# Kernel optimization log

Measured on AMD Instinct MI355X. Metric: run time of the kernel, lower is better.

## Reference

```python
import jax, jax.numpy as jnp
import numpy as np

_OFF = 8
_M = 512  # coordinate hash base (> max coord + 2*_OFF)

def _enc(c):
    c64 = c.astype(np.int64) + _OFF
    return (c64[:, 0] * _M + c64[:, 1]) * _M + c64[:, 2]

def _kmap(out_c, in_c, scale):
    """Per-offset neighbor map: maps[k, j] = index into in_c of voxel out_c[j] + scale*offset_k, or -1."""
    ik = _enc(in_c)
    order = np.argsort(ik)
    sk = ik[order]
    maps = np.full((27, len(out_c)), -1, np.int32)
    k = 0
    for dx in (-1, 0, 1):
        for dy in (-1, 0, 1):
            for dz in (-1, 0, 1):
                ck = _enc(out_c + np.array([dx, dy, dz]) * scale)
                pos = np.clip(np.searchsorted(sk, ck), 0, len(sk) - 1)
                hit = sk[pos] == ck
                maps[k] = np.where(hit, order[pos].astype(np.int32), -1)
                k += 1
    return maps


def setup_inputs() -> dict:
    rng = np.random.default_rng(0)
    c = rng.integers(0, 160, size=(300000, 3))
    c0 = np.unique(c, axis=0)[:200000]          # stride-1 voxels
    c2 = np.unique((c0 // 2) * 2, axis=0)       # stride-2 voxels
    c4 = np.unique((c2 // 4) * 4, axis=0)       # stride-4 voxels

    maps = {
        'map0':  jnp.asarray(_kmap(c0, c0, 1)),   # block0  (s=1)
        'map1':  jnp.asarray(_kmap(c2, c0, 1)),   # block1  (s=2 down)
        'map2':  jnp.asarray(_kmap(c4, c2, 2)),   # block2  (s=2 down)
        'map2t': jnp.asarray(_kmap(c2, c4, 2)),   # block2_tr (transposed)
        'map1t': jnp.asarray(_kmap(c0, c2, 1)),   # block1_tr (transposed)
        'map0t': jnp.asarray(_kmap(c0, c0, 1)),   # block0_tr (s=1)
    }

    key = jax.random.key(0)
    ks = jax.random.split(key, 8)

    def w(k, cin, cout):
        return jax.random.normal(k, (27, cin, cout), jnp.float32) / np.sqrt(27.0 * cin)

    nf, e = 16, 32
    inp = {'feats': jax.random.normal(ks[0], (c0.shape[0], nf), jnp.float32)}
    inp['W0'] = w(ks[1], nf, e);          inp['g0'] = jnp.ones((e,));        inp['b0'] = jnp.zeros((e,))
    inp['W1'] = w(ks[2], e, 2 * e);       inp['g1'] = jnp.ones((2 * e,));    inp['b1'] = jnp.zeros((2 * e,))
    inp['W2'] = w(ks[3], 2 * e, 4 * e);   inp['g2'] = jnp.ones((4 * e,));    inp['b2'] = jnp.zeros((4 * e,))
    inp['W2t'] = w(ks[4], 4 * e, 2 * e);  inp['g2t'] = jnp.ones((2 * e,));   inp['b2t'] = jnp.zeros((2 * e,))
    inp['W1t'] = w(ks[5], 4 * e, 2 * e);  inp['g1t'] = jnp.ones((2 * e,));   inp['b1t'] = jnp.zeros((2 * e,))
    inp['W0t'] = w(ks[6], 3 * e, 2)
    inp.update(maps)
    return inp


def _sconv(x, W, m):
    """Sparse 3D conv as gather-GEMM-scatter. x:[Nin,Cin], W:[27,Cin,Cout], m:[27,Nout]."""
    valid = m >= 0
    idx = jnp.maximum(m, 0)
    acc0 = jnp.zeros((m.shape[1], W.shape[2]), x.dtype)

    def body(acc, kw):
        mk, vk, Wk = kw
        g = jnp.where(vk[:, None], x[mk], 0.0)
        return acc + g @ Wk, None

    out, _ = jax.lax.scan(body, acc0, (idx, valid, W))
    return out


def _bn_relu(x, g, b, eps=1e-5):
    mu = x.mean(0)
    var = x.var(0)
    return jax.nn.relu((x - mu) * jax.lax.rsqrt(var + eps) * g + b)


def reference(feats, W0, g0, b0, W1, g1, b1, W2, g2, b2,
              W2t, g2t, b2t, W1t, g1t, b1t, W0t,
              map0, map1, map2, map2t, map1t, map0t):
    s1 = _bn_relu(_sconv(feats, W0, map0), g0, b0)   # [N0, 32]
    s2 = _bn_relu(_sconv(s1, W1, map1), g1, b1)      # [N1, 64]
    s4 = _bn_relu(_sconv(s2, W2, map2), g2, b2)      # [N2, 128]
    d2 = _bn_relu(_sconv(s4, W2t, map2t), g2t, b2t)  # [N1, 64]
    d2 = jnp.concatenate([d2, s2], axis=1)           # [N1, 128] skip cat
    d1 = _bn_relu(_sconv(d2, W1t, map1t), g1t, b1t)  # [N0, 64]
    d1 = jnp.concatenate([d1, s1], axis=1)           # [N0, 96] skip cat
    return _sconv(d1, W0t, map0t)                    # [N0, 2]
```

## Files before the change

kernel.cpp:

```cpp
#include <hip/hip_runtime.h>
#include <cstddef>
#include <cstdint>

#define BN_EPS 1e-5f

typedef float f2 __attribute__((ext_vector_type(2)));
typedef float f4 __attribute__((ext_vector_type(4)));
typedef float f32x4 __attribute__((ext_vector_type(4)));
typedef _Float16 h2 __attribute__((ext_vector_type(2)));
typedef _Float16 h8 __attribute__((ext_vector_type(8)));

__device__ __forceinline__ int xcd_swz(int bid, int nwg)
{
    const int q = nwg >> 3, r = nwg & 7;
    const int xcd = bid & 7, idx = bid >> 3;
    const int base = (xcd < r) ? xcd * (q + 1) : r * (q + 1) + (xcd - r) * q;
    return base + idx;
}

template<int CIN, int COUT>
__global__ __launch_bounds__(256)
void wtrans_mf(const float* __restrict__ W, _Float16* __restrict__ Wm)
{
    constexpr int NT = CIN / 32;
    constexpr int NC = COUT / 16;
    const int t = blockIdx.x * 256 + threadIdx.x;
    constexpr int TOTAL = 27 * NT * NC * 64;
    if (t >= TOTAL) return;
    const int lane = t & 63;
    int rest = t >> 6;
    const int ct = rest % NC; rest /= NC;
    const int tt = rest % NT;
    const int k  = rest / NT;
    const int cin0 = tt * 32 + (lane >> 4) * 8;
    const int co   = ct * 16 + (lane & 15);
    h8 v;
    #pragma unroll
    for (int u = 0; u < 8; ++u)
        v[u] = (_Float16)W[((size_t)k * CIN + cin0 + u) * COUT + co];
    *(h8*)(Wm + (size_t)t * 8) = v;
}

__global__ __launch_bounds__(256)
void wtrans_mf0(const float* __restrict__ W, _Float16* __restrict__ Wm0)
{
    const int t = blockIdx.x * 256 + threadIdx.x;
    constexpr int TOTAL = 27 * 2 * 32;
    if (t >= TOTAL) return;
    const int co = t % 32;
    const int s  = (t / 32) % 2;
    const int k  = t / 64;
    h8 v;
    #pragma unroll
    for (int u = 0; u < 8; ++u)
        v[u] = (_Float16)W[((size_t)k * 16 + s * 8 + u) * 32 + co];
    *(h8*)(Wm0 + (size_t)t * 8) = v;
}

__global__ __launch_bounds__(256)
void map_transpose_cls(const int* __restrict__ map, int Nout,
                       int* __restrict__ mapT, unsigned char* __restrict__ cls,
                       int* __restrict__ counts)
{
    __shared__ int s[256][28];
    __shared__ int hist[9];
    const int tid  = threadIdx.x;
    const int base = blockIdx.x * 256;
    const int j    = base + tid;
    if (tid < 9) hist[tid] = 0;
    for (int k = 0; k < 27; ++k)
        s[tid][k] = (j < Nout) ? map[(size_t)k * Nout + j] : -1;
    __syncthreads();
    for (int i = tid; i < 256 * 32; i += 256) {
        const int r = i >> 5, c = i & 31;
        if (base + r < Nout)
            mapT[(size_t)(base + r) * 32 + c] = (c < 27) ? s[r][c] : -1;
    }
    if (j < Nout) {
        int c9 = 8;
        #pragma unroll 1
        for (int k = 0; k < 27; ++k) {
            if (s[tid][k] >= 0) {
                const int dz = k % 3, dy = (k / 3) % 3, dx = k / 9;
                c9 = ((dx != 1) << 2) | ((dy != 1) << 1) | (int)(dz != 1);
                break;
            }
        }
        cls[j] = (unsigned char)c9;
        atomicAdd(&hist[c9], 1);
    }
    __syncthreads();
    if (tid < 9 && hist[tid] > 0)
        atomicAdd(&counts[tid], hist[tid]);
}

__global__ __launch_bounds__(256)
void scatter_compact(const unsigned char* __restrict__ cls, int Nout,
                     const int* __restrict__ counts, int* __restrict__ cursors,
                     int* __restrict__ order)
{
    __shared__ int hist[9], basec[9];
    const int tid = threadIdx.x;
    const int j   = blockIdx.x * 256 + tid;
    if (tid < 9) hist[tid] = 0;
    const int c9 = (j < Nout) ? (int)cls[j] : -1;
    __syncthreads();
    int lpos = 0;
    if (c9 >= 0) lpos = atomicAdd(&hist[c9], 1);
    __syncthreads();
    if (tid < 9 && hist[tid] > 0)
        basec[tid] = atomicAdd(&cursors[tid], hist[tid]);
    __syncthreads();
    if (c9 >= 0) {
        int offs = 0;
        #pragma unroll
        for (int c = 0; c < 9; ++c)
            if (c < c9) offs += counts[c];
        order[offs + basec[c9] + lpos] = j;
    }
}

__global__ __launch_bounds__(256)
void sconv_mf0(const float* __restrict__ x, const _Float16* __restrict__ Wm0,
               const int* __restrict__ map, int Nout,
               _Float16* __restrict__ out, const float* __restrict__ zrow)
{
    const int lane = threadIdx.x & 63;
    const int wave = threadIdx.x >> 6;
    const int row0 = (blockIdx.x * 4 + wave) * 16;

    __shared__ int smap[4][16][28];

    int mk[16];
    bool anyv = false;
    #pragma unroll
    for (int r = 0; r < 16; ++r) {
        const int j = row0 + r;
        mk[r] = (lane < 27 && j < Nout) ? map[(size_t)lane * Nout + j] : -1;
        anyv |= (mk[r] >= 0);
    }
    unsigned long long act = __ballot(anyv);

    if (lane < 27) {
        #pragma unroll
        for (int r = 0; r < 16; ++r)
            smap[wave][r][lane] = mk[r];
    }

    f32x4 accH[2], accL[2];
    #pragma unroll
    for (int c = 0; c < 2; ++c) {
        accH[c] = (f32x4){0.f, 0.f, 0.f, 0.f};
        accL[c] = (f32x4){0.f, 0.f, 0.f, 0.f};
    }

    const int rrow = lane & 15;
    const int kseg = lane >> 4;
    const int half = kseg & 1;
    const bool useK1 = (kseg < 2);

    while (act) {
        const int k1 = (int)__builtin_ctzll(act);
        act &= act - 1;
        int k2 = -1;
        if (act) {
            k2 = (int)__builtin_ctzll(act);
            act &= act - 1;
        }
        const int ks = useK1 ? k1 : k2;
        int m = -1;
        if (ks >= 0) m = smap[wave][rrow][ks];

        const float* px = (m >= 0) ? (x + (size_t)m * 16 + half * 8)
                                   : (zrow + half * 8);
        const f4 x0 = *(const f4*)px;
        const f4 x1 = *(const f4*)(px + 4);
        h8 aH, aL;
        #pragma unroll
        for (int u = 0; u < 4; ++u) {
            const float v0 = x0[u], v1 = x1[u];
            const _Float16 h0 = (_Float16)v0;
            const _Float16 h1 = (_Float16)v1;
            aH[u]     = h0;
            aH[u + 4] = h1;
            aL[u]     = (_Float16)((v0 - (float)h0) * 2048.f);
            aL[u + 4] = (_Float16)((v1 - (float)h1) * 2048.f);
        }

        const int ksafe = (ks >= 0) ? ks : 0;
        const _Float16* wb = Wm0 + ((size_t)(ksafe * 2 + half) * 32) * 8;
        #pragma unroll
        for (int c = 0; c < 2; ++c) {
            const h8 b = *(const h8*)(wb + (size_t)(c * 16 + rrow) * 8);
            accH[c] = __builtin_amdgcn_mfma_f32_16x16x32_f16(aH, b, accH[c], 0, 0, 0);
            accL[c] = __builtin_amdgcn_mfma_f32_16x16x32_f16(aL, b, accL[c], 0, 0, 0);
        }
    }

    #pragma unroll
    for (int c = 0; c < 2; ++c) {
        #pragma unroll
        for (int r = 0; r < 4; ++r) {
            const int j = row0 + kseg * 4 + r;
            if (j < Nout)
                out[(size_t)j * 32 + c * 16 + rrow] =
                    (_Float16)(accH[c][r] + accL[c][r] * (1.f / 2048.f));
        }
    }
}

template<int CIN, int CINA, int COUT>
__global__ __launch_bounds__(256)
void sconv_mf(const _Float16* __restrict__ xA, const _Float16* __restrict__ xB,
              const _Float16* __restrict__ Wm, const int* __restrict__ map,
              int Nout, _Float16* __restrict__ out,
              const _Float16* __restrict__ zrh)
{
    constexpr int CINB = CIN - CINA;
    constexpr int NT = CIN / 32;
    constexpr int NC = COUT / 16;
    static_assert(CINA % 32 == 0, "CINA must be a multiple of 32");
    const int lane = threadIdx.x & 63;
    const int wave = threadIdx.x >> 6;
    const int row0 = (blockIdx.x * 4 + wave) * 32;

    __shared__ int smap[4][32][28];

    int mv[32];
    #pragma unroll
    for (int r = 0; r < 32; ++r) {
        const int j = row0 + r;
        mv[r] = (lane < 27 && j < Nout) ? map[(size_t)lane * Nout + j] : -1;
    }
    bool anyv = false;
    #pragma unroll
    for (int r = 0; r < 32; ++r) {
        if (lane < 27) smap[wave][r][lane] = mv[r];
        anyv |= (mv[r] >= 0);
    }
    unsigned long long act = __ballot(anyv) & 0x7FFFFFFull;

    f32x4 acc[2][NC];
    #pragma unroll
    for (int tt = 0; tt < 2; ++tt)
        #pragma unroll
        for (int c = 0; c < NC; ++c) acc[tt][c] = (f32x4){0.f, 0.f, 0.f, 0.f};

    const int rrow = lane & 15;
    const int kseg = lane >> 4;

    auto loada = [&](int k, h8 a[2][NT]) {
        #pragma unroll
        for (int tt = 0; tt < 2; ++tt) {
            const int m = smap[wave][tt * 16 + rrow][k];
            #pragma unroll
            for (int t = 0; t < NT; ++t) {
                const int cin0 = t * 32 + kseg * 8;
                const _Float16* pa;
                if (m >= 0) {
                    if (CINB > 0 && t * 32 >= CINA)
                        pa = xB + (size_t)m * CINB + (cin0 - CINA);
                    else
                        pa = xA + (size_t)m * CINA + cin0;
                } else {
                    pa = zrh;
                }
                a[tt][t] = *(const h8*)pa;
            }
        }
    };
    auto compute = [&](int k, h8 a[2][NT]) {
        const _Float16* Wk = Wm + ((size_t)k * NT * NC * 64 + lane) * 8;
        #pragma unroll
        for (int t = 0; t < NT; ++t) {
            #pragma unroll
            for (int c = 0; c < NC; ++c) {
                const h8 b = *(const h8*)(Wk + (size_t)(t * NC + c) * 64 * 8);
                acc[0][c] = __builtin_amdgcn_mfma_f32_16x16x32_f16(a[0][t], b, acc[0][c], 0, 0, 0);
                acc[1][c] = __builtin_amdgcn_mfma_f32_16x16x32_f16(a[1][t], b, acc[1][c], 0, 0, 0);
            }
        }
    };

    h8 aC[2][NT], aN[2][NT];
    int kC = -1;
    if (act) {
        kC = (int)__builtin_ctzll(act);
        act &= act - 1;
        loada(kC, aC);
    }
    while (kC >= 0) {
        int kN = -1;
        if (act) {
            kN = (int)__builtin_ctzll(act);
            act &= act - 1;
            loada(kN, aN);
        }
        compute(kC, aC);
        #pragma unroll
        for (int tt = 0; tt < 2; ++tt)
            #pragma unroll
            for (int t = 0; t < NT; ++t) aC[tt][t] = aN[tt][t];
        kC = kN;
    }

    #pragma unroll
    for (int tt = 0; tt < 2; ++tt) {
        #pragma unroll
        for (int c = 0; c < NC; ++c) {
            #pragma unroll
            for (int r = 0; r < 4; ++r) {
                const int j = row0 + tt * 16 + kseg * 4 + r;
                if (j < Nout)
                    out[(size_t)j * COUT + c * 16 + rrow] = (_Float16)acc[tt][c][r];
            }
        }
    }
}

template<int CIN, int CINA, int COUT>
__global__ __launch_bounds__(256)
void sconv_mf_g(const _Float16* __restrict__ xA, const _Float16* __restrict__ xB,
                const _Float16* __restrict__ Wm, const int* __restrict__ mapT,
                const int* __restrict__ order, int Nout,
                _Float16* __restrict__ out, const _Float16* __restrict__ zrh)
{
    constexpr int CINB = CIN - CINA;
    constexpr int NT = CIN / 32;
    constexpr int NC = COUT / 16;
    static_assert(CINA % 32 == 0, "CINA must be a multiple of 32");
    const int lane = threadIdx.x & 63;
    const int wave = threadIdx.x >> 6;
    const int wrow0 = (blockIdx.x * 4 + wave) * 32;

    __shared__ int sjr[4][32];
    __shared__ int smap[4][32][28];

    int jreg = -1;
    if (lane < 32) {
        const int idx = wrow0 + lane;
        if (idx < Nout) jreg = order[idx];
    }
    if (!__ballot(jreg >= 0)) return;
    if (lane < 32) sjr[wave][lane] = jreg;

    int mv[32];
    #pragma unroll
    for (int r = 0; r < 32; ++r) {
        const int jr = __shfl(jreg, r);
        mv[r] = (jr >= 0 && lane < 27) ? mapT[(size_t)jr * 32 + lane] : -1;
    }
    bool anyv = false;
    #pragma unroll
    for (int r = 0; r < 32; ++r) {
        if (lane < 27) smap[wave][r][lane] = mv[r];
        anyv |= (mv[r] >= 0);
    }
    unsigned long long act = __ballot(anyv) & 0x7FFFFFFull;

    f32x4 acc[2][NC];
    #pragma unroll
    for (int tt = 0; tt < 2; ++tt)
        #pragma unroll
        for (int c = 0; c < NC; ++c) acc[tt][c] = (f32x4){0.f, 0.f, 0.f, 0.f};

    const int rrow = lane & 15;
    const int kseg = lane >> 4;

    auto loada = [&](int k, h8 a[2][NT]) {
        #pragma unroll
        for (int tt = 0; tt < 2; ++tt) {
            const int m = smap[wave][tt * 16 + rrow][k];
            #pragma unroll
            for (int t = 0; t < NT; ++t) {
                const int cin0 = t * 32 + kseg * 8;
                const _Float16* pa;
                if (m >= 0) {
                    if (CINB > 0 && t * 32 >= CINA)
                        pa = xB + (size_t)m * CINB + (cin0 - CINA);
                    else
                        pa = xA + (size_t)m * CINA + cin0;
                } else {
                    pa = zrh;
                }
                a[tt][t] = *(const h8*)pa;
            }
        }
    };
    auto compute = [&](int k, h8 a[2][NT]) {
        const _Float16* Wk = Wm + ((size_t)k * NT * NC * 64 + lane) * 8;
        #pragma unroll
        for (int t = 0; t < NT; ++t) {
            #pragma unroll
            for (int c = 0; c < NC; ++c) {
                const h8 b = *(const h8*)(Wk + (size_t)(t * NC + c) * 64 * 8);
                acc[0][c] = __builtin_amdgcn_mfma_f32_16x16x32_f16(a[0][t], b, acc[0][c], 0, 0, 0);
                acc[1][c] = __builtin_amdgcn_mfma_f32_16x16x32_f16(a[1][t], b, acc[1][c], 0, 0, 0);
            }
        }
    };

    h8 aC[2][NT], aN[2][NT];
    int kC = -1;
    if (act) {
        kC = (int)__builtin_ctzll(act);
        act &= act - 1;
        loada(kC, aC);
    }
    while (kC >= 0) {
        int kN = -1;
        if (act) {
            kN = (int)__builtin_ctzll(act);
            act &= act - 1;
            loada(kN, aN);
        }
        compute(kC, aC);
        #pragma unroll
        for (int tt = 0; tt < 2; ++tt)
            #pragma unroll
            for (int t = 0; t < NT; ++t) aC[tt][t] = aN[tt][t];
        kC = kN;
    }

    #pragma unroll
    for (int tt = 0; tt < 2; ++tt) {
        #pragma unroll
        for (int c = 0; c < NC; ++c) {
            #pragma unroll
            for (int r = 0; r < 4; ++r) {
                const int j = sjr[wave][tt * 16 + kseg * 4 + r];
                if (j >= 0)
                    out[(size_t)j * COUT + c * 16 + rrow] = (_Float16)acc[tt][c][r];
            }
        }
    }
}

__global__ __launch_bounds__(256)
void sconv0t(const _Float16* __restrict__ d1, const _Float16* __restrict__ s1,
             const float* __restrict__ W ,
             const int* __restrict__ map, int N, float* __restrict__ out,
             const _Float16* __restrict__ zrh)
{
    const int tid  = threadIdx.x;
    const int lane = tid & 63;
    const int l32  = tid & 31;
    const int bid  = xcd_swz(blockIdx.x, gridDim.x);
    const int j    = bid * 8 + (tid >> 5);

    int mk = (l32 < 27 && j < N) ? map[(size_t)l32 * N + j] : -1;
    const unsigned long long bal = __ballot(mk >= 0);
    unsigned int act = (unsigned int)((bal | (bal >> 32)) & 0x7FFFFFFu);

    float a0 = 0.f, a1 = 0.f;
    while (act) {
        const int k1 = (int)__builtin_ctz(act);
        act &= act - 1;
        int k2 = -1;
        if (act) { k2 = (int)__builtin_ctz(act); act &= act - 1; }
        const int k2s = (k2 >= 0) ? k2 : k1;

        const int m1 = __shfl(mk, (lane & 32) + k1);
        int m2 = __shfl(mk, (lane & 32) + k2s);
        if (k2 < 0) m2 = -1;

        const _Float16* p1a = (m1 >= 0) ? (d1 + (size_t)m1 * 64) : zrh;
        const _Float16* p1b = (m1 >= 0) ? (s1 + (size_t)m1 * 32) : zrh;
        const _Float16* p2a = (m2 >= 0) ? (d1 + (size_t)m2 * 64) : zrh;
        const _Float16* p2b = (m2 >= 0) ? (s1 + (size_t)m2 * 32) : zrh;
        const h2 xa1 = *(const h2*)(p1a + 2 * l32);
        const float xs1 = (float)p1b[l32];
        const h2 xa2 = *(const h2*)(p2a + 2 * l32);
        const float xs2 = (float)p2b[l32];

        const f4 wa1 = *(const f4*)(W + (size_t)k1 * 192 + 4 * l32);
        const f2 ws1 = *(const f2*)(W + (size_t)k1 * 192 + 128 + 2 * l32);
        const f4 wa2 = *(const f4*)(W + (size_t)k2s * 192 + 4 * l32);
        const f2 ws2 = *(const f2*)(W + (size_t)k2s * 192 + 128 + 2 * l32);

        a0 = fmaf((float)xa1[0], wa1[0], a0);
        a1 = fmaf((float)xa1[0], wa1[1], a1);
        a0 = fmaf((float)xa1[1], wa1[2], a0);
        a1 = fmaf((float)xa1[1], wa1[3], a1);
        a0 = fmaf(xs1, ws1[0], a0);
        a1 = fmaf(xs1, ws1[1], a1);

        a0 = fmaf((float)xa2[0], wa2[0], a0);
        a1 = fmaf((float)xa2[0], wa2[1], a1);
        a0 = fmaf((float)xa2[1], wa2[2], a0);
        a1 = fmaf((float)xa2[1], wa2[3], a1);
        a0 = fmaf(xs2, ws2[0], a0);
        a1 = fmaf(xs2, ws2[1], a1);
    }
    #pragma unroll
    for (int off = 1; off < 32; off <<= 1) {
        a0 += __shfl_xor(a0, off, 32);
        a1 += __shfl_xor(a1, off, 32);
    }
    if (l32 == 0 && j < N) {
        out[(size_t)j * 2 + 0] = a0;
        out[(size_t)j * 2 + 1] = a1;
    }
}

template<int C>
__global__ __launch_bounds__(256)
void bn_reduce_v(const _Float16* __restrict__ x, int N,
                 float* __restrict__ sums)
{
    constexpr int CV = C / 8;
    const int tid  = threadIdx.x;
    const int lane = tid & 63;
    const int wave = tid >> 6;
    const size_t total  = (size_t)N * CV;
    const size_t stride = (size_t)gridDim.x * 256;
    const size_t gid    = (size_t)blockIdx.x * 256 + tid;

    float s[8], s2[8];
    #pragma unroll
    for (int u = 0; u < 8; ++u) { s[u] = 0.f; s2[u] = 0.f; }

    for (size_t v = gid; v < total; v += stride) {
        const h8 hv = *(const h8*)(x + v * 8);
        #pragma unroll
        for (int u = 0; u < 8; ++u) {
            const float f = (float)hv[u];
            s[u] += f;
            s2[u] += f * f;
        }
    }

    #pragma unroll
    for (int off = CV; off < 64; off <<= 1) {
        #pragma unroll
        for (int u = 0; u < 8; ++u) {
            s[u]  += __shfl_xor(s[u], off);
            s2[u] += __shfl_xor(s2[u], off);
        }
    }

    __shared__ float shs[4][16][8];
    __shared__ float shq[4][16][8];
    if (lane < CV) {
        #pragma unroll
        for (int u = 0; u < 8; ++u) {
            shs[wave][lane][u] = s[u];
            shq[wave][lane][u] = s2[u];
        }
    }
    __syncthreads();
    if (tid < C) {
        const int ph = tid >> 3, u = tid & 7;
        float ts = 0.f, tq = 0.f;
        #pragma unroll
        for (int w = 0; w < 4; ++w) {
            ts += shs[w][ph][u];
            tq += shq[w][ph][u];
        }
        atomicAdd(&sums[tid], ts);
        atomicAdd(&sums[C + tid], tq);
    }
}

template<int C>
__global__ __launch_bounds__(256)
void bn_apply_v(_Float16* __restrict__ x, int N,
                const float* __restrict__ sums,
                const float* __restrict__ g, const float* __restrict__ b)
{
    constexpr int CV = C / 8;
    const size_t total  = (size_t)N * CV;
    const size_t stride = (size_t)gridDim.x * 256;
    const size_t gid    = (size_t)blockIdx.x * 256 + threadIdx.x;
    const int phase = (int)(gid % CV);

    const float invN = 1.0f / (float)N;
    float sc[8], sh[8];
    #pragma unroll
    for (int u = 0; u < 8; ++u) {
        const int c = phase * 8 + u;
        const float mean = sums[c] * invN;
        float var = sums[C + c] * invN - mean * mean;
        var = fmaxf(var, 0.f);
        sc[u] = g[c] * rsqrtf(var + BN_EPS);
        sh[u] = b[c] - mean * sc[u];
    }

    for (size_t v = gid; v < total; v += stride) {
        h8 hv = *(h8*)(x + v * 8);
        #pragma unroll
        for (int u = 0; u < 8; ++u) {
            const float f = fmaf((float)hv[u], sc[u], sh[u]);
            hv[u] = (_Float16)(f > 0.f ? f : 0.f);
        }
        *(h8*)(x + v * 8) = hv;
    }
}

extern "C" void kernel_launch(void* const* d_in, const int* in_sizes, int n_in,
                              void* d_out, int out_size, void* d_ws, size_t ws_size,
                              hipStream_t stream)
{
    const float* feats = (const float*)d_in[0];
    const float* W0  = (const float*)d_in[1];
    const float* g0  = (const float*)d_in[2];
    const float* b0  = (const float*)d_in[3];
    const float* W1  = (const float*)d_in[4];
    const float* g1  = (const float*)d_in[5];
    const float* b1  = (const float*)d_in[6];
    const float* W2  = (const float*)d_in[7];
    const float* g2  = (const float*)d_in[8];
    const float* b2  = (const float*)d_in[9];
    const float* W2t = (const float*)d_in[10];
    const float* g2t = (const float*)d_in[11];
    const float* b2t = (const float*)d_in[12];
    const float* W1t = (const float*)d_in[13];
    const float* g1t = (const float*)d_in[14];
    const float* b1t = (const float*)d_in[15];
    const float* W0t = (const float*)d_in[16];
    const int* map0  = (const int*)d_in[17];
    const int* map1  = (const int*)d_in[18];
    const int* map2  = (const int*)d_in[19];
    const int* map2t = (const int*)d_in[20];
    const int* map1t = (const int*)d_in[21];
    const int* map0t = (const int*)d_in[22];

    const int N0 = in_sizes[0] / 16;
    const int N1 = in_sizes[18] / 27;
    const int N2 = in_sizes[19] / 27;

    float* ws = (float*)d_ws;
    float* sums  = ws;
    float* sums0 = sums;
    float* sums1 = sums + 64;
    float* sums2 = sums + 192;
    float* sums3 = sums + 448;
    float* sums4 = sums + 576;
    float* zrow  = sums + 704;
    int*   gcnt  = (int*)(zrow + 128);
    _Float16* Wm0h = (_Float16*)(gcnt + 64);
    _Float16* Wh1  = Wm0h + 27 * 2 * 32 * 8;
    _Float16* Wh2  = Wh1 + 27 * 32 * 64;
    _Float16* Wh2t = Wh2 + 27 * 64 * 128;
    _Float16* Wh1t = Wh2t + 27 * 128 * 64;
    _Float16* y0 = Wh1t + 27 * 128 * 64;
    _Float16* y1 = y0 + (size_t)N0 * 32;
    _Float16* y2 = y1 + (size_t)N1 * 64;
    _Float16* y3 = y2 + (size_t)N2 * 128;
    _Float16* y4 = y3 + (size_t)N1 * 64;
    int* mapT = (int*)(y4 + (size_t)N0 * 64);
    int* orderA = mapT + (size_t)N0 * 32;
    int* orderB = orderA + N1;
    unsigned char* clsb = (unsigned char*)(orderB + N0);
    const _Float16* zrh = (const _Float16*)zrow;

    (void)hipMemsetAsync(sums, 0, (704 + 128 + 64) * sizeof(float), stream);

    wtrans_mf0<<<(27 * 2 * 32 + 255) / 256, 256, 0, stream>>>(W0, Wm0h);
    wtrans_mf<32, 64><<<(27 * 1 * 4 * 64 + 255) / 256, 256, 0, stream>>>(W1, Wh1);
    wtrans_mf<64, 128><<<(27 * 2 * 8 * 64 + 255) / 256, 256, 0, stream>>>(W2, Wh2);
    wtrans_mf<128, 64><<<(27 * 4 * 4 * 64 + 255) / 256, 256, 0, stream>>>(W2t, Wh2t);
    wtrans_mf<128, 64><<<(27 * 4 * 4 * 64 + 255) / 256, 256, 0, stream>>>(W1t, Wh1t);

    sconv_mf0<<<(N0 + 63) / 64, 256, 0, stream>>>(
        feats, Wm0h, map0, N0, y0, zrow);
    bn_reduce_v<32><<<512, 256, 0, stream>>>(y0, N0, sums0);
    bn_apply_v<32><<<1024, 256, 0, stream>>>(y0, N0, sums0, g0, b0);

    sconv_mf<32, 32, 64><<<(N1 + 127) / 128, 256, 0, stream>>>(
        y0, nullptr, Wh1, map1, N1, y1, zrh);
    bn_reduce_v<64><<<512, 256, 0, stream>>>(y1, N1, sums1);
    bn_apply_v<64><<<1024, 256, 0, stream>>>(y1, N1, sums1, g1, b1);

    sconv_mf<64, 64, 128><<<(N2 + 127) / 128, 256, 0, stream>>>(
        y1, nullptr, Wh2, map2, N2, y2, zrh);
    bn_reduce_v<128><<<512, 256, 0, stream>>>(y2, N2, sums2);
    bn_apply_v<128><<<1024, 256, 0, stream>>>(y2, N2, sums2, g2, b2);

    map_transpose_cls<<<(N1 + 255) / 256, 256, 0, stream>>>(
        map2t, N1, mapT, clsb, gcnt);
    scatter_compact<<<(N1 + 255) / 256, 256, 0, stream>>>(
        clsb, N1, gcnt, gcnt + 16, orderA);
    sconv_mf_g<128, 128, 64><<<(N1 + 127) / 128, 256, 0, stream>>>(
        y2, nullptr, Wh2t, mapT, orderA, N1, y3, zrh);
    bn_reduce_v<64><<<512, 256, 0, stream>>>(y3, N1, sums3);
    bn_apply_v<64><<<1024, 256, 0, stream>>>(y3, N1, sums3, g2t, b2t);

    map_transpose_cls<<<(N0 + 255) / 256, 256, 0, stream>>>(
        map1t, N0, mapT, clsb, gcnt + 32);
    scatter_compact<<<(N0 + 255) / 256, 256, 0, stream>>>(
        clsb, N0, gcnt + 32, gcnt + 48, orderB);
    sconv_mf_g<128, 64, 64><<<(N0 + 127) / 128, 256, 0, stream>>>(
        y3, y1, Wh1t, mapT, orderB, N0, y4, zrh);
    bn_reduce_v<64><<<512, 256, 0, stream>>>(y4, N0, sums4);
    bn_apply_v<64><<<1024, 256, 0, stream>>>(y4, N0, sums4, g1t, b1t);

    sconv0t<<<(N0 + 7) / 8, 256, 0, stream>>>(y4, y0, W0t, map0t, N0,
                                              (float*)d_out, zrh);
}
```

Before: 632.9 us.

## Split output channels across grid y for small-N sparse conv layers

Adds an output-channel split so each block computes only NCW of the 16-wide output column tiles, selected by blockIdx.y. The stride-4 conv (N2 small) is split four ways and the transposed block2 conv two ways, which multiplies the block count to fill more CUs and cuts per-wave accumulator registers. In exchange, each split block redoes the map load and the gather of input rows, so gather traffic goes up for those layers. The other two launches keep full width and behave as before.

```diff
diff --git a/kernel.cpp b/kernel.cpp
--- a/kernel.cpp
+++ b/kernel.cpp
@@ -209,7 +209,7 @@
     }
 }
 
-template<int CIN, int CINA, int COUT>
+template<int CIN, int CINA, int COUT, int NCW>
 __global__ __launch_bounds__(256)
 void sconv_mf(const _Float16* __restrict__ xA, const _Float16* __restrict__ xB,
               const _Float16* __restrict__ Wm, const int* __restrict__ map,
@@ -223,6 +223,7 @@
     const int lane = threadIdx.x & 63;
     const int wave = threadIdx.x >> 6;
     const int row0 = (blockIdx.x * 4 + wave) * 32;
+    const int cb   = blockIdx.y * NCW;
 
     __shared__ int smap[4][32][28];
 
@@ -240,11 +241,11 @@
     }
     unsigned long long act = __ballot(anyv) & 0x7FFFFFFull;
 
-    f32x4 acc[2][NC];
+    f32x4 acc[2][NCW];
     #pragma unroll
     for (int tt = 0; tt < 2; ++tt)
         #pragma unroll
-        for (int c = 0; c < NC; ++c) acc[tt][c] = (f32x4){0.f, 0.f, 0.f, 0.f};
+        for (int c = 0; c < NCW; ++c) acc[tt][c] = (f32x4){0.f, 0.f, 0.f, 0.f};
 
     const int rrow = lane & 15;
     const int kseg = lane >> 4;
@@ -274,8 +275,8 @@
         #pragma unroll
         for (int t = 0; t < NT; ++t) {
             #pragma unroll
-            for (int c = 0; c < NC; ++c) {
-                const h8 b = *(const h8*)(Wk + (size_t)(t * NC + c) * 64 * 8);
+            for (int c = 0; c < NCW; ++c) {
+                const h8 b = *(const h8*)(Wk + (size_t)(t * NC + cb + c) * 64 * 8);
                 acc[0][c] = __builtin_amdgcn_mfma_f32_16x16x32_f16(a[0][t], b, acc[0][c], 0, 0, 0);
                 acc[1][c] = __builtin_amdgcn_mfma_f32_16x16x32_f16(a[1][t], b, acc[1][c], 0, 0, 0);
             }
@@ -307,18 +308,18 @@
     #pragma unroll
     for (int tt = 0; tt < 2; ++tt) {
         #pragma unroll
-        for (int c = 0; c < NC; ++c) {
+        for (int c = 0; c < NCW; ++c) {
             #pragma unroll
             for (int r = 0; r < 4; ++r) {
                 const int j = row0 + tt * 16 + kseg * 4 + r;
                 if (j < Nout)
-                    out[(size_t)j * COUT + c * 16 + rrow] = (_Float16)acc[tt][c][r];
+                    out[(size_t)j * COUT + (cb + c) * 16 + rrow] = (_Float16)acc[tt][c][r];
             }
         }
     }
 }
 
-template<int CIN, int CINA, int COUT>
+template<int CIN, int CINA, int COUT, int NCW>
 __global__ __launch_bounds__(256)
 void sconv_mf_g(const _Float16* __restrict__ xA, const _Float16* __restrict__ xB,
                 const _Float16* __restrict__ Wm, const int* __restrict__ mapT,
@@ -332,6 +333,7 @@
     const int lane = threadIdx.x & 63;
     const int wave = threadIdx.x >> 6;
     const int wrow0 = (blockIdx.x * 4 + wave) * 32;
+    const int cb    = blockIdx.y * NCW;
 
     __shared__ int sjr[4][32];
     __shared__ int smap[4][32][28];
@@ -358,11 +360,11 @@
     }
     unsigned long long act = __ballot(anyv) & 0x7FFFFFFull;
 
-    f32x4 acc[2][NC];
+    f32x4 acc[2][NCW];
     #pragma unroll
     for (int tt = 0; tt < 2; ++tt)
         #pragma unroll
-        for (int c = 0; c < NC; ++c) acc[tt][c] = (f32x4){0.f, 0.f, 0.f, 0.f};
+        for (int c = 0; c < NCW; ++c) acc[tt][c] = (f32x4){0.f, 0.f, 0.f, 0.f};
 
     const int rrow = lane & 15;
     const int kseg = lane >> 4;
@@ -392,8 +394,8 @@
         #pragma unroll
         for (int t = 0; t < NT; ++t) {
             #pragma unroll
-            for (int c = 0; c < NC; ++c) {
-                const h8 b = *(const h8*)(Wk + (size_t)(t * NC + c) * 64 * 8);
+            for (int c = 0; c < NCW; ++c) {
+                const h8 b = *(const h8*)(Wk + (size_t)(t * NC + cb + c) * 64 * 8);
                 acc[0][c] = __builtin_amdgcn_mfma_f32_16x16x32_f16(a[0][t], b, acc[0][c], 0, 0, 0);
                 acc[1][c] = __builtin_amdgcn_mfma_f32_16x16x32_f16(a[1][t], b, acc[1][c], 0, 0, 0);
             }
@@ -425,12 +427,12 @@
     #pragma unroll
     for (int tt = 0; tt < 2; ++tt) {
         #pragma unroll
-        for (int c = 0; c < NC; ++c) {
+        for (int c = 0; c < NCW; ++c) {
             #pragma unroll
             for (int r = 0; r < 4; ++r) {
                 const int j = sjr[wave][tt * 16 + kseg * 4 + r];
                 if (j >= 0)
-                    out[(size_t)j * COUT + c * 16 + rrow] = (_Float16)acc[tt][c][r];
+                    out[(size_t)j * COUT + (cb + c) * 16 + rrow] = (_Float16)acc[tt][c][r];
             }
         }
     }
@@ -667,12 +669,12 @@
     bn_reduce_v<32><<<512, 256, 0, stream>>>(y0, N0, sums0);
     bn_apply_v<32><<<1024, 256, 0, stream>>>(y0, N0, sums0, g0, b0);
 
-    sconv_mf<32, 32, 64><<<(N1 + 127) / 128, 256, 0, stream>>>(
+    sconv_mf<32, 32, 64, 4><<<(N1 + 127) / 128, 256, 0, stream>>>(
         y0, nullptr, Wh1, map1, N1, y1, zrh);
     bn_reduce_v<64><<<512, 256, 0, stream>>>(y1, N1, sums1);
     bn_apply_v<64><<<1024, 256, 0, stream>>>(y1, N1, sums1, g1, b1);
 
-    sconv_mf<64, 64, 128><<<(N2 + 127) / 128, 256, 0, stream>>>(
+    sconv_mf<64, 64, 128, 2><<<dim3((N2 + 127) / 128, 4), 256, 0, stream>>>(
         y1, nullptr, Wh2, map2, N2, y2, zrh);
     bn_reduce_v<128><<<512, 256, 0, stream>>>(y2, N2, sums2);
     bn_apply_v<128><<<1024, 256, 0, stream>>>(y2, N2, sums2, g2, b2);
@@ -681,7 +683,7 @@
         map2t, N1, mapT, clsb, gcnt);
     scatter_compact<<<(N1 + 255) / 256, 256, 0, stream>>>(
         clsb, N1, gcnt, gcnt + 16, orderA);
-    sconv_mf_g<128, 128, 64><<<(N1 + 127) / 128, 256, 0, stream>>>(
+    sconv_mf_g<128, 128, 64, 2><<<dim3((N1 + 127) / 128, 2), 256, 0, stream>>>(
         y2, nullptr, Wh2t, mapT, orderA, N1, y3, zrh);
     bn_reduce_v<64><<<512, 256, 0, stream>>>(y3, N1, sums3);
     bn_apply_v<64><<<1024, 256, 0, stream>>>(y3, N1, sums3, g2t, b2t);
@@ -690,7 +692,7 @@
         map1t, N0, mapT, clsb, gcnt + 32);
     scatter_compact<<<(N0 + 255) / 256, 256, 0, stream>>>(
         clsb, N0, gcnt + 32, gcnt + 48, orderB);
-    sconv_mf_g<128, 64, 64><<<(N0 + 127) / 128, 256, 0, stream>>>(
+    sconv_mf_g<128, 64, 64, 4><<<(N0 + 127) / 128, 256, 0, stream>>>(
         y3, y1, Wh1t, mapT, orderB, N0, y4, zrh);
     bn_reduce_v<64><<<512, 256, 0, stream>>>(y4, N0, sums4);
     bn_apply_v<64><<<1024, 256, 0, stream>>>(y4, N0, sums4, g1t, b1t);
```

Measured after the change: 661.5 us. 4.5% more time.
